# Performance work log

Hardware: AMD Instinct MI355X
Metric: run time of the kernel (lower is better)

## Reference

```python
import jax, jax.numpy as jnp
import numpy as np

NEG_SLOPE = 0.2  # PyG GATConv default LeakyReLU slope


def add_self_loops(edge_index, n):
    loops = jnp.arange(n, dtype=edge_index.dtype)
    return jnp.concatenate([edge_index, jnp.stack([loops, loops])], axis=1)


def segment_softmax(e, seg, n):
    # e: [E, H], seg: [E] destination node ids
    m = jax.ops.segment_max(e, seg, num_segments=n)          # [N, H]
    ex = jnp.exp(e - m[seg])
    s = jax.ops.segment_sum(ex, seg, num_segments=n)          # [N, H]
    return ex / (s[seg] + 1e-16)


def gat_conv(x, edge_index, W, att_src, att_dst, bias, heads, concat):
    n = x.shape[0]
    c = W.shape[1] // heads
    ei = add_self_loops(edge_index, n)
    src, dst = ei[0], ei[1]
    h = (x @ W).reshape(n, heads, c)                          # [N, H, C]
    a_src = jnp.einsum('nhc,hc->nh', h, att_src)              # [N, H]
    a_dst = jnp.einsum('nhc,hc->nh', h, att_dst)
    e = a_src[src] + a_dst[dst]                               # [E, H]
    e = jax.nn.leaky_relu(e, NEG_SLOPE)
    alpha = segment_softmax(e, dst, n)                        # [E, H]
    msg = alpha[:, :, None] * h[src]                          # [E, H, C]
    out = jax.ops.segment_sum(msg, dst, num_segments=n)       # [N, H, C]
    if concat:
        out = out.reshape(n, heads * c)
    else:
        out = out.mean(axis=1)
    return out + bias


def setup_inputs() -> dict:
    key = jax.random.key(0)
    ks = jax.random.split(key, 16)
    N, E, IN, HID, H, OUT = 50000, 1600000, 512, 256, 8, 128
    s = 0.1
    return {
        'x': jax.random.normal(ks[0], (N, IN), jnp.float32),
        'edge_index': jax.random.randint(ks[1], (2, E), 0, N, jnp.int64),
        'edge_index_2': jax.random.randint(ks[2], (2, E), 0, N, jnp.int64),
        'W1': jax.random.normal(ks[3], (IN, HID * H), jnp.float32) * s,
        'att_src1': jax.random.normal(ks[4], (H, HID), jnp.float32) * s,
        'att_dst1': jax.random.normal(ks[5], (H, HID), jnp.float32) * s,
        'b1': jnp.zeros((HID * H,), jnp.float32),
        'W2': jax.random.normal(ks[6], (HID * H, OUT), jnp.float32) * s,
        'att_src2': jax.random.normal(ks[7], (1, OUT), jnp.float32) * s,
        'att_dst2': jax.random.normal(ks[8], (1, OUT), jnp.float32) * s,
        'b2': jnp.zeros((OUT,), jnp.float32),
        'W3': jax.random.normal(ks[9], (HID * H, OUT), jnp.float32) * s,
        'att_src3': jax.random.normal(ks[10], (1, OUT), jnp.float32) * s,
        'att_dst3': jax.random.normal(ks[11], (1, OUT), jnp.float32) * s,
        'b3': jnp.zeros((OUT,), jnp.float32),
    }


def reference(x, edge_index, edge_index_2, W1, att_src1, att_dst1, b1,
              W2, att_src2, att_dst2, b2, W3, att_src3, att_dst3, b3):
    # Inference mode: F.dropout and GATConv attention dropout are no-ops.
    emb = jax.nn.elu(gat_conv(x, edge_index, W1, att_src1, att_dst1, b1, heads=8, concat=True))
    x1 = gat_conv(emb, edge_index, W2, att_src2, att_dst2, b2, heads=1, concat=False)
    x2 = gat_conv(emb, edge_index_2, W3, att_src3, att_dst3, b3, heads=1, concat=False)
    logits = jax.nn.softmax(x1, axis=1)    # nn.Softmax() legacy dim -> 1 for 2D
    logits_2 = jax.nn.softmax(x2, axis=1)
    predictions = jnp.argmax(logits, axis=1)
    return (logits, logits_2, predictions)
```

## Files before the change

### kernel.cpp

```cpp
#include <hip/hip_runtime.h>
#include <hip/hip_bf16.h>
#include <math.h>

#define N_NODES 50000
#define E_EDGES 1600000
#define EP_EDGES (E_EDGES + N_NODES)
#define IN_F 512
#define HID 256
#define HEADS 8
#define OUTF 128

typedef unsigned short u16;
typedef __attribute__((ext_vector_type(8))) short short8;
typedef __attribute__((ext_vector_type(4))) float floatx4;

static __device__ __forceinline__ float eluf(float x) {
  return x > 0.f ? x : expm1f(x);
}

static __device__ __forceinline__ u16 bf16_hi(float v) {
  __hip_bfloat16 h = __float2bfloat16(v);
  return *(u16*)&h;
}
static __device__ __forceinline__ float bf16_f(u16 u) {
  __hip_bfloat16 h = *(__hip_bfloat16*)&u;
  return __bfloat162float(h);
}
static __device__ __forceinline__ void split3_bf16(float v, u16& h, u16& m, u16& l) {
  h = bf16_hi(v);
  float r1 = v - bf16_f(h);
  m = bf16_hi(r1);
  float r2 = r1 - bf16_f(m);
  l = bf16_hi(r2);
}

static __device__ __forceinline__ int clampi(int v, int n) {
  return v < 0 ? 0 : (v >= n ? n - 1 : v);
}


__global__ void k_detect(const int* __restrict__ ei, int* __restrict__ flag) {
  __shared__ int nz;
  if (threadIdx.x == 0) nz = 0;
  __syncthreads();
  for (int i = threadIdx.x; i < 4096; i += blockDim.x)
    if (ei[2 * i + 1] != 0) nz = 1;
  __syncthreads();
  if (threadIdx.x == 0) *flag = (nz ? 0 : 1);
}

__global__ void k_init_deg(int* __restrict__ deg, int n) {
  int i = blockIdx.x * 256 + threadIdx.x;
  if (i < n) deg[i] = 1;
}

__global__ void k_count(const int* __restrict__ ei, const int* __restrict__ flag,
                        int* __restrict__ deg, int E) {
  int e = blockIdx.x * 256 + threadIdx.x;
  if (e >= E) return;
  int f = *flag;
  int idx = E + e;
  int dst = clampi(ei[f ? 2 * idx : idx], N_NODES);
  atomicAdd(&deg[dst], 1);
}

__global__ __launch_bounds__(1024) void k_scan(const int* __restrict__ deg,
                                               int* __restrict__ rp, int n) {
  __shared__ int sw[16];
  __shared__ int s_run;
  int tid = threadIdx.x, lane = tid & 63, w = tid >> 6;
  if (tid == 0) s_run = 0;
  __syncthreads();
  for (int base = 0; base < n; base += 1024) {
    int i = base + tid;
    int v = (i < n) ? deg[i] : 0;
    int sv = v;
#pragma unroll
    for (int off = 1; off < 64; off <<= 1) {
      int t = __shfl_up(sv, off);
      if (lane >= off) sv += t;
    }
    if (lane == 63) sw[w] = sv;
    __syncthreads();
    if (w == 0) {
      int wsum = (lane < 16) ? sw[lane] : 0;
#pragma unroll
      for (int off = 1; off < 16; off <<= 1) {
        int t = __shfl_up(wsum, off);
        if (lane >= off) wsum += t;
      }
      if (lane < 16) sw[lane] = wsum;
    }
    __syncthreads();
    int woff = (w > 0) ? sw[w - 1] : 0;
    int run = s_run;
    if (i < n) rp[i + 1] = run + woff + sv;
    __syncthreads();
    if (tid == 1023) s_run = run + sw[15];
    __syncthreads();
  }
  if (tid == 0) rp[0] = 0;
}

__global__ void k_fill_self(const int* __restrict__ rp, int* __restrict__ wp,
                            int* __restrict__ col, int n) {
  int i = blockIdx.x * 256 + threadIdx.x;
  if (i < n) { int p = rp[i]; col[p] = i; wp[i] = p + 1; }
}

__global__ void k_fill_edges(const int* __restrict__ ei, const int* __restrict__ flag,
                             int* __restrict__ wp, int* __restrict__ col, int E) {
  int e = blockIdx.x * 256 + threadIdx.x;
  if (e >= E) return;
  int f = *flag;
  int src = clampi(ei[f ? 2 * e : e], N_NODES);
  int didx = E + e;
  int dst = clampi(ei[f ? 2 * didx : didx], N_NODES);
  int p = atomicAdd(&wp[dst], 1);
  col[p] = src;
}

__global__ void k_split3_t(const float* __restrict__ W, u16* __restrict__ H,
                           u16* __restrict__ Mv, u16* __restrict__ L,
                           int kshift, int kmask, int Nw, int total) {
  int idx = blockIdx.x * 256 + threadIdx.x;
  if (idx >= total) return;
  int n = idx >> kshift;
  int k = idx & kmask;
  u16 h, m, l;
  split3_bf16(W[(size_t)k * Nw + n], h, m, l);
  H[idx] = h;
  Mv[idx] = m;
  L[idx] = l;
}

__global__ __launch_bounds__(256) void k_watt1(
    const float* __restrict__ W1, const float* __restrict__ attS,
    const float* __restrict__ attD, float* __restrict__ watt) {
  int wid = (blockIdx.x * 256 + threadIdx.x) >> 6;
  int lane = threadIdx.x & 63;
  if (wid >= IN_F * HEADS) return;
  int k = wid >> 3, h = wid & 7;
  float4 wv = *(const float4*)&W1[(size_t)k * (HID * HEADS) + h * HID + lane * 4];
  float4 sv = *(const float4*)&attS[h * HID + lane * 4];
  float4 dv = *(const float4*)&attD[h * HID + lane * 4];
  float s = wv.x * sv.x + wv.y * sv.y + wv.z * sv.z + wv.w * sv.w;
  float d = wv.x * dv.x + wv.y * dv.y + wv.z * dv.z + wv.w * dv.w;
  for (int off = 32; off; off >>= 1) {
    s += __shfl_xor(s, off);
    d += __shfl_xor(d, off);
  }
  if (lane == 0) {
    watt[(size_t)(2 * h) * IN_F + k] = s;
    watt[(size_t)(2 * h + 1) * IN_F + k] = d;
  }
}

__global__ __launch_bounds__(256) void k_asad1(
    const float* __restrict__ x, const float* __restrict__ watt,
    float* __restrict__ asall, float* __restrict__ adall, int n) {
  int node = (blockIdx.x * 256 + threadIdx.x) >> 6;
  int lane = threadIdx.x & 63;
  if (node >= n) return;
  float4 x0 = *(const float4*)&x[(size_t)node * IN_F + lane * 8];
  float4 x1 = *(const float4*)&x[(size_t)node * IN_F + lane * 8 + 4];
  for (int h = 0; h < HEADS; ++h) {
    const float* ws = watt + (size_t)(2 * h) * IN_F + lane * 8;
    const float* wd = watt + (size_t)(2 * h + 1) * IN_F + lane * 8;
    float4 s0 = *(const float4*)ws, s1 = *(const float4*)(ws + 4);
    float4 d0 = *(const float4*)wd, d1 = *(const float4*)(wd + 4);
    float s = x0.x * s0.x + x0.y * s0.y + x0.z * s0.z + x0.w * s0.w
            + x1.x * s1.x + x1.y * s1.y + x1.z * s1.z + x1.w * s1.w;
    float d = x0.x * d0.x + x0.y * d0.y + x0.z * d0.z + x0.w * d0.w
            + x1.x * d1.x + x1.y * d1.y + x1.z * d1.z + x1.w * d1.w;
    for (int off = 32; off; off >>= 1) {
      s += __shfl_xor(s, off);
      d += __shfl_xor(d, off);
    }
    if (lane == 0) {
      asall[(size_t)h * n + node] = s;
      adall[(size_t)h * n + node] = d;
    }
  }
}


#define GBM 128
#define GBN 128
#define GBK 32

#define MFMA_BF16 __builtin_amdgcn_mfma_f32_16x16x32_bf16

__device__ __forceinline__ void gemm_epilogue(floatx4 acc[4][4], float* C,
                                              int ldc, int M, int accum,
                                              int row0, int col0, int wr,
                                              int wc, int lane) {
  int q = lane >> 4, n15 = lane & 15;
#pragma unroll
  for (int i = 0; i < 4; ++i) {
#pragma unroll
    for (int r = 0; r < 4; ++r) {
      int row = row0 + wr * 64 + i * 16 + q * 4 + r;
      if (row < M) {
#pragma unroll
        for (int j = 0; j < 4; ++j) {
          int cg = col0 + wc * 64 + j * 16 + n15;
          float v = acc[i][j][r];
          if (accum) v += C[(size_t)row * ldc + cg];
          C[(size_t)row * ldc + cg] = v;
        }
      }
    }
  }
}

__global__ __launch_bounds__(256) void gemm1_k(
    const float* __restrict__ X, int lda,
    const u16* __restrict__ Bh, const u16* __restrict__ Bm,
    const u16* __restrict__ Bl, int ldb,
    float* __restrict__ C, int ldc, int M, int K) {
  __shared__ __align__(16) u16 lds[24576];
  int tid = threadIdx.x;
  int lane = tid & 63, wave = tid >> 6;
  int wr = wave >> 1, wc = wave & 1;
  int row0 = blockIdx.x * GBM, col0 = blockIdx.y * GBN;
  floatx4 acc[4][4] = {};
  int m0 = tid >> 2, m1 = (tid + 256) >> 2;
  int q0 = tid & 3;
  int lo0 = ((m0 >> 4) * 64 + q0 * 16 + (m0 & 15)) * 8;
  int lo1 = ((m1 >> 4) * 64 + q0 * 16 + (m1 & 15)) * 8;

  for (int k0 = 0; k0 < K; k0 += GBK) {
#pragma unroll
    for (int c = 0; c < 2; ++c) {
      int m = c ? m1 : m0;
      int lo = c ? lo1 : lo0;
      int gr = row0 + m;
      float f[8];
      if (gr < M) {
        float4 f0 = *(const float4*)(X + (size_t)gr * lda + k0 + q0 * 8);
        float4 f1 = *(const float4*)(X + (size_t)gr * lda + k0 + q0 * 8 + 4);
        f[0] = f0.x; f[1] = f0.y; f[2] = f0.z; f[3] = f0.w;
        f[4] = f1.x; f[5] = f1.y; f[6] = f1.z; f[7] = f1.w;
      } else {
#pragma unroll
        for (int e = 0; e < 8; ++e) f[e] = 0.f;
      }
      short8 vh, vm, vl;
#pragma unroll
      for (int e = 0; e < 8; ++e) {
        u16 h, m2, l;
        split3_bf16(f[e], h, m2, l);
        vh[e] = (short)h; vm[e] = (short)m2; vl[e] = (short)l;
      }
      *(short8*)&lds[lo] = vh;
      *(short8*)&lds[4096 + lo] = vm;
      *(short8*)&lds[8192 + lo] = vl;
    }
#pragma unroll
    for (int c = 0; c < 2; ++c) {
      int m = c ? m1 : m0;
      int lo = c ? lo1 : lo0;
      size_t go = (size_t)(col0 + m) * ldb + k0 + q0 * 8;
      *(short8*)&lds[12288 + lo] = *(const short8*)(Bh + go);
      *(short8*)&lds[16384 + lo] = *(const short8*)(Bm + go);
      *(short8*)&lds[20480 + lo] = *(const short8*)(Bl + go);
    }
    __syncthreads();
    short8 a_h[4], a_m[4], a_l[4];
#pragma unroll
    for (int i = 0; i < 4; ++i) {
      int o = ((wr * 4 + i) * 64 + lane) * 8;
      a_h[i] = *(short8*)&lds[o];
      a_m[i] = *(short8*)&lds[4096 + o];
      a_l[i] = *(short8*)&lds[8192 + o];
    }
#pragma unroll
    for (int j = 0; j < 4; ++j) {
      int o = ((wc * 4 + j) * 64 + lane) * 8;
      short8 b_h = *(short8*)&lds[12288 + o];
      short8 b_m = *(short8*)&lds[16384 + o];
      short8 b_l = *(short8*)&lds[20480 + o];
#pragma unroll
      for (int i = 0; i < 4; ++i) {
        acc[i][j] = MFMA_BF16(a_l[i], b_h, acc[i][j], 0, 0, 0);
        acc[i][j] = MFMA_BF16(a_m[i], b_m, acc[i][j], 0, 0, 0);
        acc[i][j] = MFMA_BF16(a_h[i], b_l, acc[i][j], 0, 0, 0);
        acc[i][j] = MFMA_BF16(a_m[i], b_h, acc[i][j], 0, 0, 0);
        acc[i][j] = MFMA_BF16(a_h[i], b_m, acc[i][j], 0, 0, 0);
        acc[i][j] = MFMA_BF16(a_h[i], b_h, acc[i][j], 0, 0, 0);
      }
    }
    __syncthreads();
  }
  gemm_epilogue(acc, C, ldc, M, 0, row0, col0, wr, wc, lane);
}

__device__ __forceinline__ void gemm_core6(
    const u16* __restrict__ Ah, const u16* __restrict__ Am,
    const u16* __restrict__ Al, int lda,
    const u16* __restrict__ Bh, const u16* __restrict__ Bm,
    const u16* __restrict__ Bl, int ldb,
    float* __restrict__ C, int ldc, int M, int K, int row0, int col0,
    int accum, u16* lds) {
  int tid = threadIdx.x;
  int lane = tid & 63, wave = tid >> 6;
  int wr = wave >> 1, wc = wave & 1;
  floatx4 acc[4][4] = {};
  int m0 = tid >> 2, m1 = (tid + 256) >> 2;
  int q0 = tid & 3;
  int lo0 = ((m0 >> 4) * 64 + q0 * 16 + (m0 & 15)) * 8;
  int lo1 = ((m1 >> 4) * 64 + q0 * 16 + (m1 & 15)) * 8;
  for (int k0 = 0; k0 < K; k0 += GBK) {
#pragma unroll
    for (int c = 0; c < 2; ++c) {
      int m = c ? m1 : m0;
      int lo = c ? lo1 : lo0;
      int gr = row0 + m;
      short8 vh = {}, vm = {}, vl = {};
      if (gr < M) {
        size_t go = (size_t)gr * lda + k0 + q0 * 8;
        vh = *(const short8*)(Ah + go);
        vm = *(const short8*)(Am + go);
        vl = *(const short8*)(Al + go);
      }
      *(short8*)&lds[lo] = vh;
      *(short8*)&lds[4096 + lo] = vm;
      *(short8*)&lds[8192 + lo] = vl;
      size_t go = (size_t)(col0 + m) * ldb + k0 + q0 * 8;
      *(short8*)&lds[12288 + lo] = *(const short8*)(Bh + go);
      *(short8*)&lds[16384 + lo] = *(const short8*)(Bm + go);
      *(short8*)&lds[20480 + lo] = *(const short8*)(Bl + go);
    }
    __syncthreads();
    short8 a_h[4], a_m[4], a_l[4];
#pragma unroll
    for (int i = 0; i < 4; ++i) {
      int o = ((wr * 4 + i) * 64 + lane) * 8;
      a_h[i] = *(short8*)&lds[o];
      a_m[i] = *(short8*)&lds[4096 + o];
      a_l[i] = *(short8*)&lds[8192 + o];
    }
#pragma unroll
    for (int j = 0; j < 4; ++j) {
      int o = ((wc * 4 + j) * 64 + lane) * 8;
      short8 b_h = *(short8*)&lds[12288 + o];
      short8 b_m = *(short8*)&lds[16384 + o];
      short8 b_l = *(short8*)&lds[20480 + o];
#pragma unroll
      for (int i = 0; i < 4; ++i) {
        acc[i][j] = MFMA_BF16(a_l[i], b_h, acc[i][j], 0, 0, 0);
        acc[i][j] = MFMA_BF16(a_m[i], b_m, acc[i][j], 0, 0, 0);
        acc[i][j] = MFMA_BF16(a_h[i], b_l, acc[i][j], 0, 0, 0);
        acc[i][j] = MFMA_BF16(a_m[i], b_h, acc[i][j], 0, 0, 0);
        acc[i][j] = MFMA_BF16(a_h[i], b_m, acc[i][j], 0, 0, 0);
        acc[i][j] = MFMA_BF16(a_h[i], b_h, acc[i][j], 0, 0, 0);
      }
    }
    __syncthreads();
  }
  gemm_epilogue(acc, C, ldc, M, accum, row0, col0, wr, wc, lane);
}

__device__ __forceinline__ void gemm_core3(
    const u16* __restrict__ Ah, const u16* __restrict__ Am, int lda,
    const u16* __restrict__ Bh, const u16* __restrict__ Bm, int ldb,
    float* __restrict__ C, int ldc, int M, int K, int row0, int col0,
    int accum, u16* lds) {
  int tid = threadIdx.x;
  int lane = tid & 63, wave = tid >> 6;
  int wr = wave >> 1, wc = wave & 1;
  floatx4 acc[4][4] = {};
  int m0 = tid >> 2, m1 = (tid + 256) >> 2;
  int q0 = tid & 3;
  int lo0 = ((m0 >> 4) * 64 + q0 * 16 + (m0 & 15)) * 8;
  int lo1 = ((m1 >> 4) * 64 + q0 * 16 + (m1 & 15)) * 8;
  for (int k0 = 0; k0 < K; k0 += GBK) {
#pragma unroll
    for (int c = 0; c < 2; ++c) {
      int m = c ? m1 : m0;
      int lo = c ? lo1 : lo0;
      int gr = row0 + m;
      short8 vh = {}, vm = {};
      if (gr < M) {
        size_t go = (size_t)gr * lda + k0 + q0 * 8;
        vh = *(const short8*)(Ah + go);
        vm = *(const short8*)(Am + go);
      }
      *(short8*)&lds[lo] = vh;
      *(short8*)&lds[4096 + lo] = vm;
      size_t go = (size_t)(col0 + m) * ldb + k0 + q0 * 8;
      *(short8*)&lds[12288 + lo] = *(const short8*)(Bh + go);
      *(short8*)&lds[16384 + lo] = *(const short8*)(Bm + go);
    }
    __syncthreads();
    short8 a_h[4], a_m[4];
#pragma unroll
    for (int i = 0; i < 4; ++i) {
      int o = ((wr * 4 + i) * 64 + lane) * 8;
      a_h[i] = *(short8*)&lds[o];
      a_m[i] = *(short8*)&lds[4096 + o];
    }
#pragma unroll
    for (int j = 0; j < 4; ++j) {
      int o = ((wc * 4 + j) * 64 + lane) * 8;
      short8 b_h = *(short8*)&lds[12288 + o];
      short8 b_m = *(short8*)&lds[16384 + o];
#pragma unroll
      for (int i = 0; i < 4; ++i) {
        acc[i][j] = MFMA_BF16(a_m[i], b_h, acc[i][j], 0, 0, 0);
        acc[i][j] = MFMA_BF16(a_h[i], b_m, acc[i][j], 0, 0, 0);
        acc[i][j] = MFMA_BF16(a_h[i], b_h, acc[i][j], 0, 0, 0);
      }
    }
    __syncthreads();
  }
  gemm_epilogue(acc, C, ldc, M, accum, row0, col0, wr, wc, lane);
}

__global__ __launch_bounds__(256) void gemm23_k(
    const u16* __restrict__ Ah, const u16* __restrict__ Am,
    const u16* __restrict__ Al, int lda,
    const u16* __restrict__ B2h, const u16* __restrict__ B2m,
    const u16* __restrict__ B2l,
    const u16* __restrict__ B3h, const u16* __restrict__ B3m, int ldb,
    float* __restrict__ C2, float* __restrict__ C3, int ldc, int M, int K,
    int accum) {
  __shared__ __align__(16) u16 lds[24576];
  if (blockIdx.z == 0)
    gemm_core6(Ah, Am, Al, lda, B2h, B2m, B2l, ldb, C2, ldc, M, K,
               blockIdx.x * GBM, 0, accum, lds);
  else
    gemm_core3(Ah, Am, lda, B3h, B3m, ldb, C3, ldc, M, K,
               blockIdx.x * GBM, 0, accum, lds);
}

template <int C>
__global__ __launch_bounds__(256) void att_dot(
    const float* __restrict__ h, const float* __restrict__ attS,
    const float* __restrict__ attD, float* __restrict__ aS,
    float* __restrict__ aD, int n) {
  int node = (blockIdx.x * 256 + threadIdx.x) >> 6;
  int lane = threadIdx.x & 63;
  if (node >= n) return;
  float s = 0.f, d = 0.f;
  if (C == 256) {
    float4 hv = *(const float4*)&h[(size_t)node * C + lane * 4];
    float4 sv = *(const float4*)&attS[lane * 4];
    float4 dv = *(const float4*)&attD[lane * 4];
    s = hv.x * sv.x + hv.y * sv.y + hv.z * sv.z + hv.w * sv.w;
    d = hv.x * dv.x + hv.y * dv.y + hv.z * dv.z + hv.w * dv.w;
  } else {
    float2 hv = *(const float2*)&h[(size_t)node * C + lane * 2];
    float2 sv = *(const float2*)&attS[lane * 2];
    float2 dv = *(const float2*)&attD[lane * 2];
    s = hv.x * sv.x + hv.y * sv.y;
    d = hv.x * dv.x + hv.y * dv.y;
  }
  for (int off = 32; off; off >>= 1) {
    s += __shfl_xor(s, off);
    d += __shfl_xor(d, off);
  }
  if (lane == 0) { aS[node] = s; aD[node] = d; }
}

__global__ __launch_bounds__(256) void aggr_l1_fused(
    const int* __restrict__ rp, const int* __restrict__ col,
    const float* __restrict__ aS, const float* __restrict__ aD,
    const float* __restrict__ h, const float* __restrict__ bias,
    u16* __restrict__ embH, u16* __restrict__ embM, u16* __restrict__ embL,
    int ecol0, int ldE, int n) {
  int node = (blockIdx.x * 256 + threadIdx.x) >> 6;
  int lane = threadIdx.x & 63;
  if (node >= n) return;
  int s0 = rp[node], s1 = rp[node + 1];
  int d = s1 - s0;
  float ad = aD[node];
  float4 acc = make_float4(0.f, 0.f, 0.f, 0.f);

  if (d <= 64) {
    int c = 0;
    float e = -3.0e38f;
    if (lane < d) {
      c = clampi(col[s0 + lane], n);
      float t = aS[c] + ad;
      e = t >= 0.f ? t : 0.2f * t;
    }
    float m = e;
    for (int off = 32; off; off >>= 1) m = fmaxf(m, __shfl_xor(m, off));
    float ex = (lane < d) ? expf(e - m) : 0.f;
    float s = ex;
    for (int off = 32; off; off >>= 1) s += __shfl_xor(s, off);
    float al = ex * (1.f / (s + 1e-16f));
    int d8 = d & ~7;
    for (int j = 0; j < d8; j += 8) {
#pragma unroll
      for (int t = 0; t < 8; ++t) {
        int ct = __shfl(c, j + t);
        float at = __shfl(al, j + t);
        float4 hv = *(const float4*)&h[(size_t)ct * HID + lane * 4];
        acc.x += at * hv.x; acc.y += at * hv.y;
        acc.z += at * hv.z; acc.w += at * hv.w;
      }
    }
    if (d8 < d) {
#pragma unroll
      for (int t = 0; t < 8; ++t) {
        if (d8 + t < d) {
          int ct = __shfl(c, d8 + t);
          float at = __shfl(al, d8 + t);
          float4 hv = *(const float4*)&h[(size_t)ct * HID + lane * 4];
          acc.x += at * hv.x; acc.y += at * hv.y;
          acc.z += at * hv.z; acc.w += at * hv.w;
        }
      }
    }
  } else {
    float m = -3.0e38f;
    for (int i = s0 + lane; i < s1; i += 64) {
      float e = aS[clampi(col[i], n)] + ad;
      e = e >= 0.f ? e : 0.2f * e;
      m = fmaxf(m, e);
    }
    for (int off = 32; off; off >>= 1) m = fmaxf(m, __shfl_xor(m, off));
    float sum = 0.f;
    for (int i = s0 + lane; i < s1; i += 64) {
      float e = aS[clampi(col[i], n)] + ad;
      e = e >= 0.f ? e : 0.2f * e;
      sum += expf(e - m);
    }
    for (int off = 32; off; off >>= 1) sum += __shfl_xor(sum, off);
    float inv = 1.f / (sum + 1e-16f);
    for (int i = s0; i < s1; ++i) {
      int ci = clampi(col[i], n);
      float e = aS[ci] + ad;
      e = e >= 0.f ? e : 0.2f * e;
      float a = expf(e - m) * inv;
      float4 hv = *(const float4*)&h[(size_t)ci * HID + lane * 4];
      acc.x += a * hv.x; acc.y += a * hv.y; acc.z += a * hv.z; acc.w += a * hv.w;
    }
  }

  float4 bb = *(const float4*)&bias[lane * 4];
  float v0 = eluf(acc.x + bb.x);
  float v1 = eluf(acc.y + bb.y);
  float v2 = eluf(acc.z + bb.z);
  float v3 = eluf(acc.w + bb.w);
  ushort4 uh, um, ul;
  split3_bf16(v0, uh.x, um.x, ul.x);
  split3_bf16(v1, uh.y, um.y, ul.y);
  split3_bf16(v2, uh.z, um.z, ul.z);
  split3_bf16(v3, uh.w, um.w, ul.w);
  size_t o = (size_t)node * ldE + ecol0 + lane * 4;
  *(ushort4*)&embH[o] = uh;
  *(ushort4*)&embM[o] = um;
  *(ushort4*)&embL[o] = ul;
}

__global__ __launch_bounds__(256) void aggr_l2_fused(
    const int* __restrict__ rp, const int* __restrict__ col,
    const float* __restrict__ aS, const float* __restrict__ aD,
    const float* __restrict__ h, const float* __restrict__ bias,
    float* __restrict__ out, float* __restrict__ pred, int n) {
  int node = (blockIdx.x * 256 + threadIdx.x) >> 6;
  int lane = threadIdx.x & 63;
  if (node >= n) return;
  int s0 = rp[node], s1 = rp[node + 1];
  int d = s1 - s0;
  float ad = aD[node];
  float2 acc = make_float2(0.f, 0.f);

  if (d <= 64) {
    int c = 0;
    float e = -3.0e38f;
    if (lane < d) {
      c = clampi(col[s0 + lane], n);
      float t = aS[c] + ad;
      e = t >= 0.f ? t : 0.2f * t;
    }
    float m = e;
    for (int off = 32; off; off >>= 1) m = fmaxf(m, __shfl_xor(m, off));
    float ex = (lane < d) ? expf(e - m) : 0.f;
    float s = ex;
    for (int off = 32; off; off >>= 1) s += __shfl_xor(s, off);
    float al = ex * (1.f / (s + 1e-16f));
    int d8 = d & ~7;
    for (int j = 0; j < d8; j += 8) {
#pragma unroll
      for (int t = 0; t < 8; ++t) {
        int ct = __shfl(c, j + t);
        float at = __shfl(al, j + t);
        float2 hv = *(const float2*)&h[(size_t)ct * OUTF + lane * 2];
        acc.x += at * hv.x; acc.y += at * hv.y;
      }
    }
    if (d8 < d) {
#pragma unroll
      for (int t = 0; t < 8; ++t) {
        if (d8 + t < d) {
          int ct = __shfl(c, d8 + t);
          float at = __shfl(al, d8 + t);
          float2 hv = *(const float2*)&h[(size_t)ct * OUTF + lane * 2];
          acc.x += at * hv.x; acc.y += at * hv.y;
        }
      }
    }
  } else {
    float m = -3.0e38f;
    for (int i = s0 + lane; i < s1; i += 64) {
      float e = aS[clampi(col[i], n)] + ad;
      e = e >= 0.f ? e : 0.2f * e;
      m = fmaxf(m, e);
    }
    for (int off = 32; off; off >>= 1) m = fmaxf(m, __shfl_xor(m, off));
    float sum = 0.f;
    for (int i = s0 + lane; i < s1; i += 64) {
      float e = aS[clampi(col[i], n)] + ad;
      e = e >= 0.f ? e : 0.2f * e;
      sum += expf(e - m);
    }
    for (int off = 32; off; off >>= 1) sum += __shfl_xor(sum, off);
    float inv = 1.f / (sum + 1e-16f);
    for (int i = s0; i < s1; ++i) {
      int ci = clampi(col[i], n);
      float e = aS[ci] + ad;
      e = e >= 0.f ? e : 0.2f * e;
      float a = expf(e - m) * inv;
      float2 hv = *(const float2*)&h[(size_t)ci * OUTF + lane * 2];
      acc.x += a * hv.x; acc.y += a * hv.y;
    }
  }

  float2 bb = *(const float2*)&bias[lane * 2];
  acc.x += bb.x; acc.y += bb.y;

  float bv;
  int bi;
  if (acc.y > acc.x) { bv = acc.y; bi = 2 * lane + 1; }
  else               { bv = acc.x; bi = 2 * lane; }
  for (int off = 32; off; off >>= 1) {
    float ov = __shfl_xor(bv, off);
    int oi = __shfl_xor(bi, off);
    if (ov > bv || (ov == bv && oi < bi)) { bv = ov; bi = oi; }
  }
  float e0 = expf(acc.x - bv), e1 = expf(acc.y - bv);
  float ssum = e0 + e1;
  for (int off = 32; off; off >>= 1) ssum += __shfl_xor(ssum, off);
  float2 r;
  r.x = e0 / ssum;
  r.y = e1 / ssum;
  *(float2*)&out[(size_t)node * OUTF + lane * 2] = r;
  if (pred != nullptr && lane == 0) pred[node] = (float)bi;
}

extern "C" void kernel_launch(void* const* d_in, const int* in_sizes, int n_in,
                              void* d_out, int out_size, void* d_ws, size_t ws_size,
                              hipStream_t stream) {
  const int N = N_NODES, E = E_EDGES;
  const float* x     = (const float*)d_in[0];
  const int*   ei1   = (const int*)d_in[1];
  const int*   ei2   = (const int*)d_in[2];
  const float* W1    = (const float*)d_in[3];
  const float* attS1 = (const float*)d_in[4];
  const float* attD1 = (const float*)d_in[5];
  const float* b1    = (const float*)d_in[6];
  const float* W2    = (const float*)d_in[7];
  const float* attS2 = (const float*)d_in[8];
  const float* attD2 = (const float*)d_in[9];
  const float* b2    = (const float*)d_in[10];
  const float* W3    = (const float*)d_in[11];
  const float* attS3 = (const float*)d_in[12];
  const float* attD3 = (const float*)d_in[13];
  const float* b3    = (const float*)d_in[14];

  size_t embPer = (size_t)N * HID * 2;
  size_t fixedBytes =
      2 * ((size_t)EP_EDGES * 4 + 256) + 2 * ((size_t)(N + 1) * 4 + 256) +
      2 * ((size_t)N * 4 + 256) + 512 +
      ((size_t)N * HID * 4 + 256) +
      ((size_t)N * OUTF * 4 * 2 + 256) +
      3 * ((size_t)IN_F * HID * HEADS * 2 + 256) +
      6 * ((size_t)HID * HEADS * OUTF * 2 + 256) +
      2 * ((size_t)HEADS * N * 4 + 256) +
      4 * ((size_t)N * 4 + 256) +
      ((size_t)2 * HEADS * IN_F * 4 + 256) +
      (1 << 20);
  int g = (ws_size >= fixedBytes + 3 * 2 * embPer) ? 2 : 1;

  char* ws = (char*)d_ws;
  size_t off = 0;
  auto take = [&](size_t bytes) {
    off = (off + 255) & ~(size_t)255;
    size_t o = off;
    off += bytes;
    return o;
  };
  int*   col1 = (int*)(ws + take((size_t)EP_EDGES * 4));
  int*   col2 = (int*)(ws + take((size_t)EP_EDGES * 4));
  int*   rp1  = (int*)(ws + take((size_t)(N + 1) * 4));
  int*   rp2  = (int*)(ws + take((size_t)(N + 1) * 4));
  int*   wp1  = (int*)(ws + take((size_t)N * 4));
  int*   wp2  = (int*)(ws + take((size_t)N * 4));
  int*   flag = (int*)(ws + take(256));
  float* h1h  = (float*)(ws + take((size_t)N * HID * 4));
  u16*   embH = (u16*)(ws + take(embPer * g));
  u16*   embM = (u16*)(ws + take(embPer * g));
  u16*   embL = (u16*)(ws + take(embPer * g));
  float* h2   = (float*)(ws + take((size_t)N * OUTF * 4 * 2));
  float* h3   = h2 + (size_t)N * OUTF;
  u16*   W1Th = (u16*)(ws + take((size_t)IN_F * HID * HEADS * 2));
  u16*   W1Tm = (u16*)(ws + take((size_t)IN_F * HID * HEADS * 2));
  u16*   W1Tl = (u16*)(ws + take((size_t)IN_F * HID * HEADS * 2));
  u16*   W2Th = (u16*)(ws + take((size_t)HID * HEADS * OUTF * 2));
  u16*   W2Tm = (u16*)(ws + take((size_t)HID * HEADS * OUTF * 2));
  u16*   W2Tl = (u16*)(ws + take((size_t)HID * HEADS * OUTF * 2));
  u16*   W3Th = (u16*)(ws + take((size_t)HID * HEADS * OUTF * 2));
  u16*   W3Tm = (u16*)(ws + take((size_t)HID * HEADS * OUTF * 2));
  u16*   W3Tl = (u16*)(ws + take((size_t)HID * HEADS * OUTF * 2));
  float* asall = (float*)(ws + take((size_t)HEADS * N * 4));
  float* adall = (float*)(ws + take((size_t)HEADS * N * 4));
  float* as2  = (float*)(ws + take((size_t)N * 4));
  float* ad2  = (float*)(ws + take((size_t)N * 4));
  float* as3  = (float*)(ws + take((size_t)N * 4));
  float* ad3  = (float*)(ws + take((size_t)N * 4));
  float* watt = (float*)(ws + take((size_t)2 * HEADS * IN_F * 4));

  float* outp = (float*)d_out;
  float* x1   = outp;
  float* x2   = outp + (size_t)N * OUTF;
  float* pred = outp + (size_t)2 * N * OUTF;

  const int gN = (N + 255) / 256;
  const int gE = (E + 255) / 256;
  const int gW = (N + 3) / 4;
  const int gM = (N + GBM - 1) / GBM;

  k_split3_t<<<(IN_F * HID * HEADS + 255) / 256, 256, 0, stream>>>(
      W1, W1Th, W1Tm, W1Tl, 9, 511, HID * HEADS, IN_F * HID * HEADS);
  k_split3_t<<<(HID * HEADS * OUTF + 255) / 256, 256, 0, stream>>>(
      W2, W2Th, W2Tm, W2Tl, 11, 2047, OUTF, HID * HEADS * OUTF);
  k_split3_t<<<(HID * HEADS * OUTF + 255) / 256, 256, 0, stream>>>(
      W3, W3Th, W3Tm, W3Tl, 11, 2047, OUTF, HID * HEADS * OUTF);

  k_watt1<<<(IN_F * HEADS * 64 + 255) / 256, 256, 0, stream>>>(
      W1, attS1, attD1, watt);
  k_asad1<<<gW, 256, 0, stream>>>(x, watt, asall, adall, N);

  k_detect<<<1, 256, 0, stream>>>(ei1, flag);

  k_init_deg<<<gN, 256, 0, stream>>>(wp1, N);
  k_count<<<gE, 256, 0, stream>>>(ei1, flag, wp1, E);
  k_scan<<<1, 1024, 0, stream>>>(wp1, rp1, N);
  k_fill_self<<<gN, 256, 0, stream>>>(rp1, wp1, col1, N);
  k_fill_edges<<<gE, 256, 0, stream>>>(ei1, flag, wp1, col1, E);

  k_init_deg<<<gN, 256, 0, stream>>>(wp2, N);
  k_count<<<gE, 256, 0, stream>>>(ei2, flag, wp2, E);
  k_scan<<<1, 1024, 0, stream>>>(wp2, rp2, N);
  k_fill_self<<<gN, 256, 0, stream>>>(rp2, wp2, col2, N);
  k_fill_edges<<<gE, 256, 0, stream>>>(ei2, flag, wp2, col2, E);

  const int ldE = g * HID;
  for (int h = 0; h < HEADS; ++h) {
    gemm1_k<<<dim3(gM, HID / GBN), 256, 0, stream>>>(
        x, IN_F,
        W1Th + (size_t)h * HID * IN_F, W1Tm + (size_t)h * HID * IN_F,
        W1Tl + (size_t)h * HID * IN_F, IN_F, h1h, HID, N, IN_F);
    aggr_l1_fused<<<gW, 256, 0, stream>>>(
        rp1, col1, asall + (size_t)h * N, adall + (size_t)h * N, h1h,
        b1 + (size_t)h * HID, embH, embM, embL, (h % g) * HID, ldE, N);
    if ((h % g) == g - 1) {
      int h0 = h - (g - 1);
      gemm23_k<<<dim3(gM, 1, 2), 256, 0, stream>>>(
          embH, embM, embL, ldE,
          W2Th + (size_t)h0 * HID, W2Tm + (size_t)h0 * HID,
          W2Tl + (size_t)h0 * HID,
          W3Th + (size_t)h0 * HID, W3Tm + (size_t)h0 * HID, HID * HEADS,
          h2, h3, OUTF, N, ldE, h0 > 0 ? 1 : 0);
    }
  }

  att_dot<OUTF><<<gW, 256, 0, stream>>>(h2, attS2, attD2, as2, ad2, N);
  att_dot<OUTF><<<gW, 256, 0, stream>>>(h3, attS3, attD3, as3, ad3, N);
  aggr_l2_fused<<<gW, 256, 0, stream>>>(rp1, col1, as2, ad2, h2, b2, x1, pred, N);
  aggr_l2_fused<<<gW, 256, 0, stream>>>(rp2, col2, as3, ad3, h3, b3, x2, nullptr, N);
}
```

Measured before the change: 4.137 ms.

## Software-pipeline per-head GEMMs with aggregation in one fused launch

Replaces the per-head sequence of gemm1, aggregation and gemm23 launches with a single fused kernel per head. That kernel interleaves GEMM tiles for the next head's projection and the previous head's layer-2/3 GEMM with this head's edge aggregation blocks, using double-buffered h1 and emb buffers. The aim is to overlap compute-bound MFMA work with memory-bound gather work and to cut launch serialization. In exchange it needs more workspace, falls back to unpipelined per-head launches when workspace is short, and shares LDS sizing across the block types.

```diff
diff --git a/kernel.cpp b/kernel.cpp
--- a/kernel.cpp
+++ b/kernel.cpp
@@ -184,10 +184,10 @@
   }
 }
 
-
 #define GBM 128
 #define GBN 128
 #define GBK 32
+#define GM1 391
 
 #define MFMA_BF16 __builtin_amdgcn_mfma_f32_16x16x32_bf16
 
@@ -214,16 +214,15 @@
   }
 }
 
-__global__ __launch_bounds__(256) void gemm1_k(
+__device__ __forceinline__ void gemm1_core(
     const float* __restrict__ X, int lda,
     const u16* __restrict__ Bh, const u16* __restrict__ Bm,
     const u16* __restrict__ Bl, int ldb,
-    float* __restrict__ C, int ldc, int M, int K) {
-  __shared__ __align__(16) u16 lds[24576];
+    float* __restrict__ C, int ldc, int M, int K, int row0, int col0,
+    u16* lds) {
   int tid = threadIdx.x;
   int lane = tid & 63, wave = tid >> 6;
   int wr = wave >> 1, wc = wave & 1;
-  int row0 = blockIdx.x * GBM, col0 = blockIdx.y * GBN;
   floatx4 acc[4][4] = {};
   int m0 = tid >> 2, m1 = (tid + 256) >> 2;
   int q0 = tid & 3;
@@ -294,6 +293,16 @@
     __syncthreads();
   }
   gemm_epilogue(acc, C, ldc, M, 0, row0, col0, wr, wc, lane);
+}
+
+__global__ __launch_bounds__(256) void gemm1_k(
+    const float* __restrict__ X, int lda,
+    const u16* __restrict__ Bh, const u16* __restrict__ Bm,
+    const u16* __restrict__ Bl, int ldb,
+    float* __restrict__ C, int ldc, int M, int K) {
+  __shared__ __align__(16) u16 lds[24576];
+  gemm1_core(X, lda, Bh, Bm, Bl, ldb, C, ldc, M, K,
+             blockIdx.x * GBM, blockIdx.y * GBN, lds);
 }
 
 __device__ __forceinline__ void gemm_core6(
@@ -464,15 +473,13 @@
   if (lane == 0) { aS[node] = s; aD[node] = d; }
 }
 
-__global__ __launch_bounds__(256) void aggr_l1_fused(
+static __device__ __forceinline__ void aggr_l1_core(
+    int node, int lane,
     const int* __restrict__ rp, const int* __restrict__ col,
     const float* __restrict__ aS, const float* __restrict__ aD,
     const float* __restrict__ h, const float* __restrict__ bias,
     u16* __restrict__ embH, u16* __restrict__ embM, u16* __restrict__ embL,
     int ecol0, int ldE, int n) {
-  int node = (blockIdx.x * 256 + threadIdx.x) >> 6;
-  int lane = threadIdx.x & 63;
-  if (node >= n) return;
   int s0 = rp[node], s1 = rp[node + 1];
   int d = s1 - s0;
   float ad = aD[node];
@@ -555,6 +562,65 @@
   *(ushort4*)&embH[o] = uh;
   *(ushort4*)&embM[o] = um;
   *(ushort4*)&embL[o] = ul;
+}
+
+__global__ __launch_bounds__(256) void aggr_l1_fused(
+    const int* __restrict__ rp, const int* __restrict__ col,
+    const float* __restrict__ aS, const float* __restrict__ aD,
+    const float* __restrict__ h, const float* __restrict__ bias,
+    u16* __restrict__ embH, u16* __restrict__ embM, u16* __restrict__ embL,
+    int ecol0, int ldE, int n) {
+  int node = (blockIdx.x * 256 + threadIdx.x) >> 6;
+  int lane = threadIdx.x & 63;
+  if (node >= n) return;
+  aggr_l1_core(node, lane, rp, col, aS, aD, h, bias, embH, embM, embL,
+               ecol0, ldE, n);
+}
+
+__global__ __launch_bounds__(256) void fused_step(
+    const int* __restrict__ rp, const int* __restrict__ col,
+    const float* __restrict__ aS, const float* __restrict__ aD,
+    const float* __restrict__ hg, const float* __restrict__ bias,
+    u16* __restrict__ embH, u16* __restrict__ embM, u16* __restrict__ embL,
+    int ecol0, int ldE, int n,
+    const float* __restrict__ X,
+    const u16* __restrict__ B1h, const u16* __restrict__ B1m,
+    const u16* __restrict__ B1l, float* __restrict__ h1out, int nG1,
+    const u16* __restrict__ A23h, const u16* __restrict__ A23m,
+    const u16* __restrict__ A23l,
+    const u16* __restrict__ B2h, const u16* __restrict__ B2m,
+    const u16* __restrict__ B2l,
+    const u16* __restrict__ B3h, const u16* __restrict__ B3m,
+    float* __restrict__ C2, float* __restrict__ C3, int accum, int nG23) {
+  __shared__ __align__(16) u16 lds[24576];
+  int nC = nG1 + nG23;
+  int k = blockIdx.x;
+  int q = k / 9, r = k - q * 9;
+  if (r == 0 && q < nC) {
+    if (q < nG1) {
+      int bx = q % GM1, by = q / GM1;
+      gemm1_core(X, IN_F, B1h, B1m, B1l, IN_F, h1out, HID, n, IN_F,
+                 bx * GBM, by * GBN, lds);
+    } else {
+      int p = q - nG1;
+      int z = p / GM1, bx = p - z * GM1;
+      if (z == 0)
+        gemm_core6(A23h, A23m, A23l, ldE, B2h, B2m, B2l, HID * HEADS,
+                   C2, OUTF, n, HID, bx * GBM, 0, accum, lds);
+      else
+        gemm_core3(A23h, A23m, ldE, B3h, B3m, HID * HEADS,
+                   C3, OUTF, n, HID, bx * GBM, 0, accum, lds);
+    }
+    return;
+  }
+  int skipped = q + (r ? 1 : 0);
+  if (skipped > nC) skipped = nC;
+  int aggrIdx = k - skipped;
+  int node = aggrIdx * 4 + (threadIdx.x >> 6);
+  int lane = threadIdx.x & 63;
+  if (node >= n) return;
+  aggr_l1_core(node, lane, rp, col, aS, aD, hg, bias, embH, embM, embL,
+               ecol0, ldE, n);
 }
 
 __global__ __launch_bounds__(256) void aggr_l2_fused(
@@ -673,19 +739,21 @@
   const float* attD3 = (const float*)d_in[13];
   const float* b3    = (const float*)d_in[14];
 
-  size_t embPer = (size_t)N * HID * 2;
-  size_t fixedBytes =
-      2 * ((size_t)EP_EDGES * 4 + 256) + 2 * ((size_t)(N + 1) * 4 + 256) +
-      2 * ((size_t)N * 4 + 256) + 512 +
-      ((size_t)N * HID * 4 + 256) +
-      ((size_t)N * OUTF * 4 * 2 + 256) +
-      3 * ((size_t)IN_F * HID * HEADS * 2 + 256) +
-      6 * ((size_t)HID * HEADS * OUTF * 2 + 256) +
-      2 * ((size_t)HEADS * N * 4 + 256) +
-      4 * ((size_t)N * 4 + 256) +
-      ((size_t)2 * HEADS * IN_F * 4 + 256) +
-      (1 << 20);
-  int g = (ws_size >= fixedBytes + 3 * 2 * embPer) ? 2 : 1;
+  size_t needPipe =
+      2 * ((size_t)EP_EDGES * 4) + 2 * ((size_t)(N + 1) * 4) +
+      2 * ((size_t)N * 4) + 4096 +
+      2 * ((size_t)N * HID * 4) +
+      3 * ((size_t)N * 512 * 2) +
+      (size_t)N * OUTF * 4 * 2 +
+      3 * ((size_t)IN_F * HID * HEADS * 2) +
+      6 * ((size_t)HID * HEADS * OUTF * 2) +
+      2 * ((size_t)HEADS * N * 4) +
+      4 * ((size_t)N * 4) +
+      (size_t)2 * HEADS * IN_F * 4 +
+      (size_t)(8 << 20);
+  int pipe = (ws_size >= needPipe) ? 1 : 0;
+  const int nbuf = pipe ? 2 : 1;
+  const int ldE = pipe ? 512 : 256;
 
   char* ws = (char*)d_ws;
   size_t off = 0;
@@ -702,10 +770,11 @@
   int*   wp1  = (int*)(ws + take((size_t)N * 4));
   int*   wp2  = (int*)(ws + take((size_t)N * 4));
   int*   flag = (int*)(ws + take(256));
-  float* h1h  = (float*)(ws + take((size_t)N * HID * 4));
-  u16*   embH = (u16*)(ws + take(embPer * g));
-  u16*   embM = (u16*)(ws + take(embPer * g));
-  u16*   embL = (u16*)(ws + take(embPer * g));
+  float* h1hA = (float*)(ws + take((size_t)N * HID * 4 * nbuf));
+  float* h1hB = pipe ? h1hA + (size_t)N * HID : h1hA;
+  u16*   embH = (u16*)(ws + take((size_t)N * ldE * 2));
+  u16*   embM = (u16*)(ws + take((size_t)N * ldE * 2));
+  u16*   embL = (u16*)(ws + take((size_t)N * ldE * 2));
   float* h2   = (float*)(ws + take((size_t)N * OUTF * 4 * 2));
   float* h3   = h2 + (size_t)N * OUTF;
   u16*   W1Th = (u16*)(ws + take((size_t)IN_F * HID * HEADS * 2));
@@ -733,7 +802,6 @@
   const int gN = (N + 255) / 256;
   const int gE = (E + 255) / 256;
   const int gW = (N + 3) / 4;
-  const int gM = (N + GBM - 1) / GBM;
 
   k_split3_t<<<(IN_F * HID * HEADS + 255) / 256, 256, 0, stream>>>(
       W1, W1Th, W1Tm, W1Tl, 9, 511, HID * HEADS, IN_F * HID * HEADS);
@@ -760,23 +828,51 @@
   k_fill_self<<<gN, 256, 0, stream>>>(rp2, wp2, col2, N);
   k_fill_edges<<<gE, 256, 0, stream>>>(ei2, flag, wp2, col2, E);
 
-  const int ldE = g * HID;
-  for (int h = 0; h < HEADS; ++h) {
-    gemm1_k<<<dim3(gM, HID / GBN), 256, 0, stream>>>(
-        x, IN_F,
-        W1Th + (size_t)h * HID * IN_F, W1Tm + (size_t)h * HID * IN_F,
-        W1Tl + (size_t)h * HID * IN_F, IN_F, h1h, HID, N, IN_F);
-    aggr_l1_fused<<<gW, 256, 0, stream>>>(
-        rp1, col1, asall + (size_t)h * N, adall + (size_t)h * N, h1h,
-        b1 + (size_t)h * HID, embH, embM, embL, (h % g) * HID, ldE, N);
-    if ((h % g) == g - 1) {
-      int h0 = h - (g - 1);
-      gemm23_k<<<dim3(gM, 1, 2), 256, 0, stream>>>(
+  if (pipe) {
+    float* buf[2] = {h1hA, h1hB};
+    gemm1_k<<<dim3(GM1, 2), 256, 0, stream>>>(
+        x, IN_F, W1Th, W1Tm, W1Tl, IN_F, buf[0], HID, N, IN_F);
+    for (int h = 0; h < HEADS; ++h) {
+      int nG1 = (h + 1 < HEADS) ? GM1 * 2 : 0;
+      int nG23 = (h >= 1) ? GM1 * 2 : 0;
+      int nC = nG1 + nG23;
+      int T = gW + nC;
+      if (9 * nC > T) T = 9 * nC;
+      int hn = (h + 1 < HEADS) ? h + 1 : h;
+      int hp = (h >= 1) ? h - 1 : 0;
+      int sp = hp & 1;
+      fused_step<<<T, 256, 0, stream>>>(
+          rp1, col1, asall + (size_t)h * N, adall + (size_t)h * N,
+          buf[h & 1], b1 + (size_t)h * HID,
+          embH, embM, embL, (h & 1) * HID, ldE, N,
+          x, W1Th + (size_t)hn * HID * IN_F, W1Tm + (size_t)hn * HID * IN_F,
+          W1Tl + (size_t)hn * HID * IN_F, buf[(h + 1) & 1], nG1,
+          embH + sp * HID, embM + sp * HID, embL + sp * HID,
+          W2Th + (size_t)hp * HID, W2Tm + (size_t)hp * HID,
+          W2Tl + (size_t)hp * HID,
+          W3Th + (size_t)hp * HID, W3Tm + (size_t)hp * HID,
+          h2, h3, hp > 0 ? 1 : 0, nG23);
+    }
+    gemm23_k<<<dim3(GM1, 1, 2), 256, 0, stream>>>(
+        embH + HID, embM + HID, embL + HID, ldE,
+        W2Th + (size_t)7 * HID, W2Tm + (size_t)7 * HID, W2Tl + (size_t)7 * HID,
+        W3Th + (size_t)7 * HID, W3Tm + (size_t)7 * HID, HID * HEADS,
+        h2, h3, OUTF, N, HID, 1);
+  } else {
+    for (int h = 0; h < HEADS; ++h) {
+      gemm1_k<<<dim3(GM1, 2), 256, 0, stream>>>(
+          x, IN_F,
+          W1Th + (size_t)h * HID * IN_F, W1Tm + (size_t)h * HID * IN_F,
+          W1Tl + (size_t)h * HID * IN_F, IN_F, h1hA, HID, N, IN_F);
+      aggr_l1_fused<<<gW, 256, 0, stream>>>(
+          rp1, col1, asall + (size_t)h * N, adall + (size_t)h * N, h1hA,
+          b1 + (size_t)h * HID, embH, embM, embL, 0, ldE, N);
+      gemm23_k<<<dim3(GM1, 1, 2), 256, 0, stream>>>(
           embH, embM, embL, ldE,
-          W2Th + (size_t)h0 * HID, W2Tm + (size_t)h0 * HID,
-          W2Tl + (size_t)h0 * HID,
-          W3Th + (size_t)h0 * HID, W3Tm + (size_t)h0 * HID, HID * HEADS,
-          h2, h3, OUTF, N, ldE, h0 > 0 ? 1 : 0);
+          W2Th + (size_t)h * HID, W2Tm + (size_t)h * HID,
+          W2Tl + (size_t)h * HID,
+          W3Th + (size_t)h * HID, W3Tm + (size_t)h * HID, HID * HEADS,
+          h2, h3, OUTF, N, HID, h > 0 ? 1 : 0);
     }
   }
 
```

Result: faster. 3.993 ms, median of 2 (-3.5%).
